# Kernel optimization log

Measured on AMD Instinct MI355X. Metric: run time of the kernel, lower is better.

The kernel has to match this reference:

```python
import jax, jax.numpy as jnp
import numpy as np

N, L, S, E, A, D = 16, 256, 128, 128, 9, 768
ARG_ROLES = 23      # score width = ARG_ROLES + 1
MAX_ARG = 9         # hard-coded max_len_arg in the torch module
N_HID = 768


def setup_inputs() -> dict:
    key = jax.random.key(0)
    ks = jax.random.split(key, 10)
    all_embeddings = jax.random.normal(ks[0], (N, L, D), jnp.float32)
    # last-3-layer BERT attention maps, 12 heads, positive entries
    attn_last3 = jax.random.uniform(ks[1], (3, N, 12, L, L), jnp.float32)
    # per-sample sorted distinct first-subword indices (all positive, full length:
    # the ragged filter idxs>0 then keeps everything -> fixed-shape gather)
    idx_keys = jax.random.split(ks[2], N)
    cand = jnp.arange(1, L - MAX_ARG - 1)
    idxs_to_collect = jax.vmap(
        lambda k: jnp.sort(jax.random.choice(k, cand, (S + 2,), replace=False))
    )(idx_keys).astype(jnp.int32)
    is_triggers = (jax.random.uniform(ks[3], (N, S)) < 0.05).astype(jnp.float32)
    is_triggers = is_triggers.at[:, 0].set(1.0)  # >=1 trigger per sample
    entity_mapping = jax.random.normal(ks[4], (N, S, E), jnp.float32) * 0.05
    arg_weight_matrices = jax.random.normal(ks[5], (N, MAX_ARG, A), jnp.float32) * 0.3
    map_keys = jax.random.split(ks[6], N)
    arg_mapping = jax.vmap(
        lambda k: jax.random.permutation(k, ARG_ROLES + 1)[:A]
    )(map_keys).astype(jnp.int32)
    W1 = jax.random.normal(ks[7], (6 * D, N_HID), jnp.float32) * 0.02
    b1 = jnp.zeros((N_HID,), jnp.float32)
    W2 = jax.random.normal(ks[8], (N_HID, 1), jnp.float32) * 0.02
    b2 = jnp.zeros((1,), jnp.float32)
    return {
        "all_embeddings": all_embeddings,
        "attn_last3": attn_last3,
        "entity_mapping": entity_mapping,
        "arg_weight_matrices": arg_weight_matrices,
        "is_triggers": is_triggers,
        "W1": W1, "b1": b1, "W2": W2, "b2": b2,
        "idxs_to_collect": idxs_to_collect,
        "arg_mapping": arg_mapping,
    }


def reference(all_embeddings, attn_last3, entity_mapping, arg_weight_matrices,
              is_triggers, W1, b1, W2, b2, idxs_to_collect, arg_mapping):
    sqrt_d = jnp.sqrt(jnp.asarray(D, jnp.float32))
    sent_idx = idxs_to_collect[:, :S]                      # [N,S] first-subword ids
    # get_fist_subword_embeddings: ragged gather (full-length here)
    sent_emb = jnp.take_along_axis(all_embeddings, sent_idx[:, :, None], axis=1)  # [N,S,D]
    # arg-type tokens sit right after the second-to-last [SEP]
    arg_pos = idxs_to_collect[:, -2:-1] + 1 + jnp.arange(MAX_ARG)[None, :]        # [N,9]
    arg_raw = jnp.take_along_axis(all_embeddings, arg_pos[:, :, None], axis=1)    # [N,9,D]

    entity_emb = jnp.einsum('nsd,nse->ned', sent_emb, entity_mapping)             # [N,E,D]
    trig = jnp.sum(sent_emb * is_triggers[..., None], axis=1) \
           / jnp.sum(is_triggers, axis=1, keepdims=True)                          # [N,D]
    del trig  # _trigger is computed but unused downstream in the torch forward
    arg_emb = jnp.einsum('nkd,nka->nad', arg_raw, arg_weight_matrices)            # [N,A,D]

    # bi-attention scores (broadcast-mul-sum == contraction over D)
    t2a = jnp.einsum('ned,nad->nea', entity_emb, arg_emb) / sqrt_d
    w = (t2a - 5.0) / 2.0                                                         # [N,E,A]
    token_argAwared = jnp.einsum('nea,nad->ned', w, arg_emb)                      # [N,E,D]
    arg_tokenAwared = jnp.einsum('nea,ned->nad', w, entity_emb)                   # [N,A,D]

    # select_hidden_att for each of the last 3 layers
    att_mean = jnp.mean(attn_last3, axis=2)                                       # [3,N,L,L]
    def sel_layer(a):  # a: [N,L,L] -> row/col gather + row renorm
        s = jax.vmap(lambda m, i: m[i][:, i])(a, sent_idx)                        # [N,S,S]
        return s / (jnp.sum(s, axis=-1, keepdims=True) + 1e-9)
    t2t = (sel_layer(att_mean[0]) + sel_layer(att_mean[1]) + sel_layer(att_mean[2])) / 3.0

    h2h_sent = jnp.einsum('nst,ntd->nsd', t2t, sent_emb)                          # [N,S,D]
    # A_h2h and H_ are projected from sent space (S) to entity space (E)
    A_h2h_e = jnp.einsum('nsd,nse->ned', h2h_sent, entity_mapping)                # [N,E,D]
    H_e = entity_emb                                                              # sent_emb projected == entity_emb

    a2a = jax.nn.softmax(jnp.einsum('nad,nbd->nab', arg_emb, arg_emb), axis=-1)   # [N,A,A]
    u2u = jnp.einsum('nab,nbd->nad', a2a, arg_emb)                                # [N,A,D]

    shp = (N, E, A, D)
    H_    = jnp.broadcast_to(H_e[:, :, None, :], shp)
    U_    = jnp.broadcast_to(arg_emb[:, None, :, :], shp)
    A_h2u = jnp.broadcast_to(token_argAwared[:, :, None, :], shp)
    A_h2h = jnp.broadcast_to(A_h2h_e[:, :, None, :], shp)
    A_u2h = jnp.broadcast_to(arg_tokenAwared[:, None, :, :], shp)
    A_u2u = jnp.broadcast_to(u2u[:, None, :, :], shp)
    latent = jnp.concatenate([H_, U_, A_h2u, A_h2h, A_u2h, A_u2u], axis=-1)       # [N,E,A,6D]

    hid = jax.nn.gelu(latent @ W1 + b1, approximate=False)                        # [N,E,A,768]
    score = (hid @ W2 + b2)[..., 0]                                               # [N,E,A]

    # map_arg_to_ids: scatter each arg slot back to its global role id
    def scatter_one(s, ids):  # s [E,A], ids [A]
        return jnp.full((E, ARG_ROLES + 1), -1e6, jnp.float32).at[:, ids].set(s)
    new_score = jax.vmap(scatter_one)(score, arg_mapping)                         # [N,E,24]
    return new_score
```

## Files before the change

kernel.cpp:

```cpp
#include <hip/hip_runtime.h>
#include <math.h>

namespace {
constexpr int N_ = 16, L_ = 256, S_ = 128, E_ = 128, A_ = 9, D_ = 768, H_ = 768, RO_ = 24;
constexpr int IDXW = 130;
constexpr int W1R = 6 * D_;
constexpr float INV_SQRT_D = 0.03608439182435161f;
constexpr int PESZ = 2048 * 768;
constexpr int PASZ = 144 * 768;
constexpr int GB_T2T    = 0;
constexpr int GB_W1T    = 1024;
constexpr int GB_GATHER = 1888;
constexpr int GB_ENTMAP = 2080;
constexpr int GB_ARGU   = 2112;
constexpr int GB_TOTAL  = 2128;
}

using bshort8 = __attribute__((ext_vector_type(8))) short;
using f32x4v = __attribute__((ext_vector_type(4))) float;

__device__ __forceinline__ unsigned short f2bf(float f) {
    unsigned u = __builtin_bit_cast(unsigned, f);
    return (unsigned short)((u + 0x7fffu + ((u >> 16) & 1u)) >> 16);
}

__device__ __forceinline__ float erf_fast(float x) {
    const float ax = fabsf(x);
    const float t = 1.0f / fmaf(0.3275911f, ax, 1.0f);
    float p = fmaf(1.061405429f, t, -1.453152027f);
    p = fmaf(p, t, 1.421413741f);
    p = fmaf(p, t, -0.284496736f);
    p = fmaf(p, t, 0.254829592f);
    p = p * t;
    const float r = 1.0f - p * __expf(-ax * ax);
    return copysignf(r, x);
}

__device__ __forceinline__ void gemm_body128(const unsigned short* __restrict__ A,
                                             const unsigned short* __restrict__ BT,
                                             int lda, int ldb, int c0, int tid,
                                             short (*As)[40], short (*Bs)[40],
                                             f32x4v acc[2][4]) {
    const int wave = tid >> 6, lane = tid & 63;
    const int row16 = lane & 15, quad = lane >> 4;
    for (int k0 = 0; k0 < S_; k0 += 32) {
#pragma unroll
        for (int i = 0; i < 2; ++i) {
            const int idx = tid + 256 * i;
            const int r = idx >> 2, q = idx & 3;
            *reinterpret_cast<bshort8*>(&As[r][q * 8]) =
                *reinterpret_cast<const bshort8*>(A + (size_t)r * lda + k0 + q * 8);
        }
        {
            const int col = tid >> 2, q = tid & 3;
            *reinterpret_cast<bshort8*>(&Bs[col][q * 8]) =
                *reinterpret_cast<const bshort8*>(BT + (size_t)(c0 + col) * ldb + k0 + q * 8);
        }
        __syncthreads();
        bshort8 a[2], b[4];
#pragma unroll
        for (int mi = 0; mi < 2; ++mi)
            a[mi] = *reinterpret_cast<const bshort8*>(&As[wave * 32 + mi * 16 + row16][quad * 8]);
#pragma unroll
        for (int ni = 0; ni < 4; ++ni)
            b[ni] = *reinterpret_cast<const bshort8*>(&Bs[ni * 16 + row16][quad * 8]);
#pragma unroll
        for (int mi = 0; mi < 2; ++mi)
#pragma unroll
            for (int ni = 0; ni < 4; ++ni)
                acc[mi][ni] = __builtin_amdgcn_mfma_f32_16x16x32_bf16(a[mi], b[ni], acc[mi][ni], 0, 0, 0);
        __syncthreads();
    }
}

__global__ __launch_bounds__(256) void stage1_k(const float* __restrict__ all_emb,
                                                const int* __restrict__ idxs,
                                                const float* __restrict__ ent_map,
                                                const float* __restrict__ W1,
                                                const float* __restrict__ argw,
                                                const float* __restrict__ attn,
                                                unsigned short* __restrict__ sentT,
                                                unsigned short* __restrict__ entmapT,
                                                short* __restrict__ W1t,
                                                unsigned short* __restrict__ t2tT,
                                                float* __restrict__ argE,
                                                unsigned short* __restrict__ argEbf,
                                                unsigned short* __restrict__ u2ubf) {
    __shared__ __align__(16) unsigned char smem[16896];
    const int b = blockIdx.x, tid = threadIdx.x;

    if (b < GB_W1T) {
        const int idx = b - GB_T2T;
        const int n = idx >> 6;
        const int half = tid >> 7, t128 = tid & 127;
        const int s0 = (idx & 63) << 1;
        const int s = s0 | half;
        const int w = t128 >> 6, lane = tid & 63;
        float* sum2 = (float*)smem;
        float* part = (float*)(smem + 12288);
        unsigned short* tileT = (unsigned short*)(smem + 12544);
        const int is = idxs[n * IDXW + s], it = idxs[n * IDXW + t128];
#pragma unroll
        for (int l = 0; l < 3; ++l) {
            const float* base = attn + ((size_t)((l * N_ + n) * 12 + w * 6)) * (L_ * L_)
                              + (size_t)is * L_ + lane * 4;
            float4 acc = {0.f, 0.f, 0.f, 0.f};
#pragma unroll
            for (int h = 0; h < 6; ++h) {
                const float4 v = *reinterpret_cast<const float4*>(base + (size_t)h * (L_ * L_));
                acc.x += v.x; acc.y += v.y; acc.z += v.z; acc.w += v.w;
            }
            *reinterpret_cast<float4*>(&sum2[(((half * 3 + l) * 2 + w) << 8) + lane * 4]) = acc;
        }
        __syncthreads();
        float m[3];
#pragma unroll
        for (int l = 0; l < 3; ++l) {
            m[l] = (sum2[(((half * 3 + l) * 2 + 0) << 8) + it] +
                    sum2[(((half * 3 + l) * 2 + 1) << 8) + it]) * (1.0f / 12.0f);
            float r = m[l];
#pragma unroll
            for (int off = 32; off; off >>= 1) r += __shfl_xor(r, off, 64);
            if (lane == 0) part[(half * 3 + l) * 2 + w] = r;
        }
        __syncthreads();
        float o = 0.f;
#pragma unroll
        for (int l = 0; l < 3; ++l)
            o += m[l] / (part[(half * 3 + l) * 2 + 0] + part[(half * 3 + l) * 2 + 1] + 1e-9f);
        tileT[t128 * 2 + half] = f2bf(o * (1.0f / 3.0f));
        __syncthreads();
        if (tid < 128) {
            const unsigned int v = ((const unsigned int*)tileT)[tid];
            *reinterpret_cast<unsigned int*>(t2tT + ((size_t)(n * S_) + tid) * S_ + s0) = v;
        }
    } else if (b < GB_GATHER) {
        const int b2 = b - GB_W1T;
        const int k0 = (b2 % 72) * 64, h0 = (b2 / 72) * 64;
        auto tile = (float (*)[65])smem;
        const int tx = tid & 63, ty = tid >> 6;
#pragma unroll
        for (int i = 0; i < 16; ++i) {
            const int r = ty + i * 4;
            tile[r][tx] = W1[(size_t)(k0 + r) * H_ + h0 + tx];
        }
        __syncthreads();
#pragma unroll
        for (int i = 0; i < 16; ++i) {
            const int r = ty + i * 4;
            W1t[(size_t)(h0 + r) * W1R + k0 + tx] = (short)f2bf(tile[tx][r]);
        }
    } else if (b < GB_ENTMAP) {
        const int b2 = b - GB_GATHER;
        const int n = b2 / 12, d0 = (b2 % 12) * 64;
        auto tile = (unsigned short (*)[132])smem;
#pragma unroll
        for (int it = 0; it < 8; ++it) {
            const int lin = tid + 256 * it;
            const int s = lin >> 4, dq = (lin & 15) * 4;
            const int row = idxs[n * IDXW + s];
            const float4 v = *reinterpret_cast<const float4*>(all_emb + ((size_t)(n * L_ + row)) * D_ + d0 + dq);
            tile[dq + 0][s] = f2bf(v.x); tile[dq + 1][s] = f2bf(v.y);
            tile[dq + 2][s] = f2bf(v.z); tile[dq + 3][s] = f2bf(v.w);
        }
        __syncthreads();
#pragma unroll
        for (int it = 0; it < 8; ++it) {
            const int lin = tid + 256 * it;
            const int d = lin >> 5, s4 = (lin & 31) * 4;
            ushort4 v = {tile[d][s4], tile[d][s4 + 1], tile[d][s4 + 2], tile[d][s4 + 3]};
            *reinterpret_cast<ushort4*>(sentT + ((size_t)(n * D_) + d0 + d) * S_ + s4) = v;
        }
    } else if (b < GB_ARGU) {
        const int idx = b - GB_ENTMAP;
        const int n = idx >> 1, e0 = (idx & 1) * 64;
        auto tile = (unsigned short (*)[132])smem;
#pragma unroll
        for (int it = 0; it < 8; ++it) {
            const int lin = tid + 256 * it;
            const int s = lin >> 4, eq = (lin & 15) * 4;
            const float4 v = *reinterpret_cast<const float4*>(ent_map + ((size_t)(n * S_ + s)) * E_ + e0 + eq);
            tile[eq + 0][s] = f2bf(v.x); tile[eq + 1][s] = f2bf(v.y);
            tile[eq + 2][s] = f2bf(v.z); tile[eq + 3][s] = f2bf(v.w);
        }
        __syncthreads();
#pragma unroll
        for (int it = 0; it < 8; ++it) {
            const int lin = tid + 256 * it;
            const int e = lin >> 5, s4 = (lin & 31) * 4;
            ushort4 v = {tile[e][s4], tile[e][s4 + 1], tile[e][s4 + 2], tile[e][s4 + 3]};
            *reinterpret_cast<ushort4*>(entmapT + ((size_t)(n * E_) + e0 + e) * S_ + s4) = v;
        }
    } else {
        const int n = b - GB_ARGU;
        auto wsm = (float (*)[A_])smem;
        auto part45 = (float (*)[4])(smem + 512);
        auto Psm = (float (*)[A_])(smem + 1536);
        if (tid < A_ * A_) wsm[tid / A_][tid % A_] = argw[n * A_ * A_ + tid];
        __syncthreads();
        const int p0 = idxs[n * IDXW + S_] + 1;
        float pp[45] = {};
        float vals[3][A_];
#pragma unroll
        for (int c = 0; c < 3; ++c) {
            const int d = tid + 256 * c;
            float raw[A_];
#pragma unroll
            for (int k = 0; k < A_; ++k) raw[k] = all_emb[((size_t)(n * L_ + p0 + k)) * D_ + d];
#pragma unroll
            for (int a = 0; a < A_; ++a) {
                float acc = 0.f;
#pragma unroll
                for (int k = 0; k < A_; ++k) acc = fmaf(raw[k], wsm[k][a], acc);
                vals[c][a] = acc;
                argE[((size_t)(n * A_ + a)) * D_ + d] = acc;
                argEbf[((size_t)(n * A_ + a)) * D_ + d] = f2bf(acc);
            }
            int p = 0;
#pragma unroll
            for (int a = 0; a < A_; ++a)
#pragma unroll
                for (int bb = a; bb < A_; ++bb) pp[p++] += vals[c][a] * vals[c][bb];
        }
        const int lane = tid & 63, wv = tid >> 6;
#pragma unroll
        for (int p = 0; p < 45; ++p) {
            float v = pp[p];
            for (int off = 32; off; off >>= 1) v += __shfl_down(v, off, 64);
            if (lane == 0) part45[p][wv] = v;
        }
        __syncthreads();
        if (tid < 45) part45[tid][0] = part45[tid][0] + part45[tid][1] + part45[tid][2] + part45[tid][3];
        __syncthreads();
        if (tid < A_) {
            const int a = tid;
            float v[A_], mx = -1e30f;
#pragma unroll
            for (int bb = 0; bb < A_; ++bb) {
                const int lo = a < bb ? a : bb, hi = a < bb ? bb : a;
                v[bb] = part45[lo * (19 - lo) / 2 + hi - lo][0];
                mx = fmaxf(mx, v[bb]);
            }
            float sm = 0.f;
#pragma unroll
            for (int bb = 0; bb < A_; ++bb) { v[bb] = expf(v[bb] - mx); sm += v[bb]; }
            const float inv = 1.0f / sm;
#pragma unroll
            for (int bb = 0; bb < A_; ++bb) Psm[a][bb] = v[bb] * inv;
        }
        __syncthreads();
#pragma unroll
        for (int c = 0; c < 3; ++c) {
            const int d = tid + 256 * c;
#pragma unroll
            for (int a = 0; a < A_; ++a) {
                float acc = 0.f;
#pragma unroll
                for (int bb = 0; bb < A_; ++bb) acc = fmaf(Psm[a][bb], vals[c][bb], acc);
                u2ubf[((size_t)(n * A_ + a)) * D_ + d] = f2bf(acc);
            }
        }
    }
}

__global__ __launch_bounds__(256) void gemm_pair_k(const unsigned short* __restrict__ entmapT,
                                                   const unsigned short* __restrict__ sentT,
                                                   const unsigned short* __restrict__ t2tT,
                                                   float* __restrict__ entf,
                                                   unsigned short* __restrict__ entbf,
                                                   unsigned short* __restrict__ M1bf) {
    __shared__ __align__(16) short As[128][40];
    __shared__ __align__(16) short Bs[64][40];
    const int bx = blockIdx.x, tid = threadIdx.x;
    const int wave = tid >> 6, lane = tid & 63;
    const int row16 = lane & 15, quad = lane >> 4;
    f32x4v acc[2][4] = {};
    if (bx < 192) {
        const int n = bx / 12, c0 = (bx % 12) * 64;
        gemm_body128(entmapT + (size_t)n * S_ * S_, sentT + (size_t)n * D_ * S_,
                     S_, S_, c0, tid, As, Bs, acc);
#pragma unroll
        for (int mi = 0; mi < 2; ++mi)
#pragma unroll
            for (int ni = 0; ni < 4; ++ni) {
                const int rbase = wave * 32 + mi * 16 + quad * 4;
                const int col = c0 + ni * 16 + row16;
#pragma unroll
                for (int t = 0; t < 4; ++t) {
                    const size_t o = ((size_t)(n * S_) + rbase + t) * D_ + col;
                    entf[o] = acc[mi][ni][t];
                    entbf[o] = f2bf(acc[mi][ni][t]);
                }
            }
    } else {
        const int idx = bx - 192;
        const int n = idx >> 1, c0 = (idx & 1) * 64;
        gemm_body128(entmapT + (size_t)n * S_ * S_, t2tT + (size_t)n * S_ * S_,
                     S_, S_, c0, tid, As, Bs, acc);
#pragma unroll
        for (int mi = 0; mi < 2; ++mi)
#pragma unroll
            for (int ni = 0; ni < 4; ++ni) {
                const int rbase = wave * 32 + mi * 16 + quad * 4;
                const int col = c0 + ni * 16 + row16;
#pragma unroll
                for (int t = 0; t < 4; ++t)
                    M1bf[((size_t)(n * S_) + rbase + t) * S_ + col] = f2bf(acc[mi][ni][t]);
            }
    }
}

__global__ __launch_bounds__(256) void gemm2_k(const unsigned short* __restrict__ M1bf,
                                               const unsigned short* __restrict__ sentT,
                                               const unsigned short* __restrict__ entbf,
                                               const unsigned short* __restrict__ argEbf,
                                               unsigned short* __restrict__ Ah2hbf,
                                               float* __restrict__ wbuf) {
    const int bx = blockIdx.x, tid = threadIdx.x;
    const int wave = tid >> 6, lane = tid & 63;
    const int row16 = lane & 15, quad = lane >> 4;
    if (bx < 192) {
        __shared__ __align__(16) short As[128][40];
        __shared__ __align__(16) short Bs[64][40];
        const int n = bx / 12, c0 = (bx % 12) * 64;
        f32x4v acc[2][4] = {};
        gemm_body128(M1bf + (size_t)n * S_ * S_, sentT + (size_t)n * D_ * S_,
                     S_, S_, c0, tid, As, Bs, acc);
#pragma unroll
        for (int mi = 0; mi < 2; ++mi)
#pragma unroll
            for (int ni = 0; ni < 4; ++ni) {
                const int rbase = wave * 32 + mi * 16 + quad * 4;
                const int col = c0 + ni * 16 + row16;
#pragma unroll
                for (int t = 0; t < 4; ++t)
                    Ah2hbf[((size_t)(n * S_) + rbase + t) * D_ + col] = f2bf(acc[mi][ni][t]);
            }
    } else {
        const int n = bx - 192;
        const unsigned short* Aent = entbf + (size_t)n * E_ * D_;
        const unsigned short* Barg = argEbf + (size_t)n * A_ * D_;
        f32x4v acc[2] = {};
        for (int k0 = 0; k0 < D_; k0 += 32) {
            bshort8 a[2], bb;
#pragma unroll
            for (int mi = 0; mi < 2; ++mi)
                a[mi] = *reinterpret_cast<const bshort8*>(Aent + (size_t)(wave * 32 + mi * 16 + row16) * D_ + k0 + quad * 8);
            bb = *reinterpret_cast<const bshort8*>(Barg + (size_t)row16 * D_ + k0 + quad * 8);
#pragma unroll
            for (int mi = 0; mi < 2; ++mi)
                acc[mi] = __builtin_amdgcn_mfma_f32_16x16x32_bf16(a[mi], bb, acc[mi], 0, 0, 0);
        }
        if (row16 < A_) {
#pragma unroll
            for (int mi = 0; mi < 2; ++mi)
#pragma unroll
                for (int t = 0; t < 4; ++t) {
                    const int e = wave * 32 + mi * 16 + quad * 4 + t;
                    const float w = (acc[mi][t] * INV_SQRT_D - 5.0f) * 0.5f;
                    wbuf[((size_t)(n * E_ + e)) * A_ + row16] = w;
                }
        }
    }
}

__global__ __launch_bounds__(256) void post_k(const float* __restrict__ wbuf,
                                              const float* __restrict__ argE,
                                              const float* __restrict__ entf,
                                              unsigned short* __restrict__ tokAbf,
                                              unsigned short* __restrict__ argTbf) {
    const int b = blockIdx.x, tid = threadIdx.x;
    if (b < N_ * E_) {
        const int n = b >> 7, e = b & 127;
        __shared__ float wl[A_];
        if (tid < A_) wl[tid] = wbuf[(size_t)(n * E_ + e) * A_ + tid];
        __syncthreads();
        const float* ar = argE + (size_t)n * A_ * D_;
#pragma unroll
        for (int c = 0; c < 3; ++c) {
            const int d = tid + 256 * c;
            float s = 0.f;
#pragma unroll
            for (int a = 0; a < A_; ++a) s = fmaf(wl[a], ar[(size_t)a * D_ + d], s);
            tokAbf[((size_t)(n * E_ + e)) * D_ + d] = f2bf(s);
        }
    } else {
        const int idx = b - N_ * E_;
        const int n = idx / A_, a = idx % A_;
        __shared__ float wl[E_];
        if (tid < E_) wl[tid] = wbuf[(size_t)(n * E_ + tid) * A_ + a];
        __syncthreads();
        const float* eb = entf + (size_t)n * E_ * D_;
#pragma unroll
        for (int c = 0; c < 3; ++c) {
            const int d = tid + 256 * c;
            float acc = 0.f;
            for (int e = 0; e < E_; ++e) acc = fmaf(wl[e], eb[(size_t)e * D_ + d], acc);
            argTbf[((size_t)(n * A_ + a)) * D_ + d] = f2bf(acc);
        }
    }
}

__global__ __launch_bounds__(256) void mfma_mlp_k(const unsigned short* __restrict__ e0,
                                                  const unsigned short* __restrict__ e1,
                                                  const unsigned short* __restrict__ e2,
                                                  const unsigned short* __restrict__ a0,
                                                  const unsigned short* __restrict__ a1,
                                                  const unsigned short* __restrict__ a2,
                                                  const short* __restrict__ W1t,
                                                  float* __restrict__ Pe3, float* __restrict__ Pa3) {
    __shared__ __align__(16) short As[128][40];
    __shared__ __align__(16) short Bs[64][40];
    const int bx = blockIdx.x;
    const int seg = bx % 3;
    const int blk = bx / 3;
    const bool isPa = blk >= 16;
    const unsigned short* Aseg;
    int woff;
    if (isPa) {
        Aseg = seg == 0 ? a0 : (seg == 1 ? a1 : a2);
        woff = seg == 0 ? 1 * D_ : (seg == 1 ? 4 * D_ : 5 * D_);
    } else {
        Aseg = seg == 0 ? e0 : (seg == 1 ? e1 : e2);
        woff = seg == 0 ? 0 : (seg == 1 ? 2 * D_ : 3 * D_);
    }
    const int M = isPa ? N_ * A_ : N_ * E_;
    const int r0 = (isPa ? blk - 16 : blk) * 128;
    float* C = isPa ? (Pa3 + (size_t)seg * PASZ) : (Pe3 + (size_t)seg * PESZ);
    const int c0 = blockIdx.y * 64;
    const int tid = threadIdx.x;
    const int wave = tid >> 6, lane = tid & 63;
    const int row16 = lane & 15, quad = lane >> 4;
    f32x4v acc[2][4] = {};
    for (int kk = 0; kk < D_; kk += 32) {
#pragma unroll
        for (int i = 0; i < 2; ++i) {
            const int idx = tid + 256 * i;
            const int r = idx >> 2, q = idx & 3;
            bshort8 av = {};
            if (r0 + r < M) av = *reinterpret_cast<const bshort8*>(Aseg + (size_t)(r0 + r) * D_ + kk + q * 8);
            *reinterpret_cast<bshort8*>(&As[r][q * 8]) = av;
        }
        {
            const int col = tid >> 2, q = tid & 3;
            *reinterpret_cast<bshort8*>(&Bs[col][q * 8]) =
                *reinterpret_cast<const bshort8*>(W1t + (size_t)(c0 + col) * W1R + woff + kk + q * 8);
        }
        __syncthreads();
        bshort8 a[2], b[4];
#pragma unroll
        for (int mi = 0; mi < 2; ++mi)
            a[mi] = *reinterpret_cast<const bshort8*>(&As[wave * 32 + mi * 16 + row16][quad * 8]);
#pragma unroll
        for (int ni = 0; ni < 4; ++ni)
            b[ni] = *reinterpret_cast<const bshort8*>(&Bs[ni * 16 + row16][quad * 8]);
#pragma unroll
        for (int mi = 0; mi < 2; ++mi)
#pragma unroll
            for (int ni = 0; ni < 4; ++ni)
                acc[mi][ni] = __builtin_amdgcn_mfma_f32_16x16x32_bf16(a[mi], b[ni], acc[mi][ni], 0, 0, 0);
        __syncthreads();
    }
#pragma unroll
    for (int mi = 0; mi < 2; ++mi) {
#pragma unroll
        for (int ni = 0; ni < 4; ++ni) {
            const int rbase = r0 + wave * 32 + mi * 16 + quad * 4;
            const int col = c0 + ni * 16 + row16;
#pragma unroll
            for (int t = 0; t < 4; ++t)
                if (rbase + t < M) C[(size_t)(rbase + t) * H_ + col] = acc[mi][ni][t];
        }
    }
}

__global__ __launch_bounds__(256) void score_k(const float* __restrict__ Pe3, const float* __restrict__ Pa3,
                                               const float* __restrict__ b1, const float* __restrict__ W2,
                                               const float* __restrict__ b2, const int* __restrict__ arg_map,
                                               float* __restrict__ out) {
    const int n = blockIdx.x >> 7, e = blockIdx.x & 127;
    const int tid = threadIdx.x;
    __shared__ float paS[A_ * H_];
    __shared__ float part[A_][4];
    float* orow = out + ((size_t)(n * E_ + e)) * RO_;
    if (tid < RO_) orow[tid] = -1000000.0f;
    for (int i = tid; i < A_ * H_; i += 256) {
        const size_t o = (size_t)n * A_ * H_ + i;
        paS[i] = Pa3[o] + Pa3[PASZ + o] + Pa3[2 * PASZ + o];
    }
    __syncthreads();
    const size_t ro = ((size_t)(n * E_ + e)) * H_;
    float acc[A_] = {};
    for (int h = tid; h < H_; h += 256) {
        const float pe = Pe3[ro + h] + Pe3[PESZ + ro + h] + Pe3[2 * PESZ + ro + h] + b1[h];
        const float w2 = W2[h];
#pragma unroll
        for (int a = 0; a < A_; ++a) {
            const float x = pe + paS[a * H_ + h];
            const float g = x * 0.5f * (1.0f + erf_fast(x * 0.70710678118654752f));
            acc[a] = fmaf(g, w2, acc[a]);
        }
    }
    const int lane = tid & 63, wv = tid >> 6;
#pragma unroll
    for (int a = 0; a < A_; ++a)
        for (int off = 32; off; off >>= 1) acc[a] += __shfl_down(acc[a], off, 64);
    if (lane == 0)
        for (int a = 0; a < A_; ++a) part[a][wv] = acc[a];
    __syncthreads();
    if (tid < A_) {
        const float s = part[tid][0] + part[tid][1] + part[tid][2] + part[tid][3] + b2[0];
        orow[arg_map[n * A_ + tid]] = s;
    }
}

extern "C" void kernel_launch(void* const* d_in, const int* in_sizes, int n_in,
                              void* d_out, int out_size, void* d_ws, size_t ws_size,
                              hipStream_t stream) {
    const float* all_emb = (const float*)d_in[0];
    const float* attn    = (const float*)d_in[1];
    const float* ent_map = (const float*)d_in[2];
    const float* argw    = (const float*)d_in[3];
    const float* W1 = (const float*)d_in[5];
    const float* b1 = (const float*)d_in[6];
    const float* W2 = (const float*)d_in[7];
    const float* b2 = (const float*)d_in[8];
    const int* idxs    = (const int*)d_in[9];
    const int* arg_map = (const int*)d_in[10];
    float* out = (float*)d_out;

    float* ws = (float*)d_ws;
    float* entf = ws + 0;
    float* Pe3  = ws + 1572864;
    float* argE = ws + 6291456;
    float* wbuf = ws + 6402048;
    float* Pa3  = ws + 6420480;
    short*          W1t     = (short*)(ws + 6752256);
    unsigned short* sentT   = (unsigned short*)(ws + 8521728);
    unsigned short* entmapT = (unsigned short*)(ws + 9308160);
    unsigned short* t2tT    = (unsigned short*)(ws + 9439232);
    unsigned short* M1bf    = (unsigned short*)(ws + 9570304);
    unsigned short* argEbf  = (unsigned short*)(ws + 9701376);
    unsigned short* u2ubf   = (unsigned short*)(ws + 9756672);
    unsigned short* entbf   = (unsigned short*)(ws + 9811968);
    unsigned short* Ah2hbf  = (unsigned short*)(ws + 10598400);
    unsigned short* tokAbf  = (unsigned short*)(ws + 11384832);
    unsigned short* argTbf  = (unsigned short*)(ws + 12171264);

    stage1_k<<<GB_TOTAL, 256, 0, stream>>>(all_emb, idxs, ent_map, W1, argw, attn,
                                           sentT, entmapT, W1t, t2tT, argE, argEbf, u2ubf);

    gemm_pair_k<<<224, 256, 0, stream>>>(entmapT, sentT, t2tT, entf, entbf, M1bf);

    gemm2_k<<<208, 256, 0, stream>>>(M1bf, sentT, entbf, argEbf, Ah2hbf, wbuf);

    post_k<<<N_ * E_ + N_ * A_, 256, 0, stream>>>(wbuf, argE, entf, tokAbf, argTbf);

    mfma_mlp_k<<<dim3(54, H_ / 64), 256, 0, stream>>>(entbf, tokAbf, Ah2hbf, argEbf, argTbf, u2ubf, W1t, Pe3, Pa3);

    score_k<<<N_ * E_, 256, 0, stream>>>(Pe3, Pa3, b1, W2, b2, arg_map, out);

    (void)in_sizes; (void)n_in; (void)out_size; (void)ws_size;
}
```

Measured before the change: 319.8 us.

## Reassociate token-arg-aware MLP term to avoid materializing tokA activations

The token_argAwared segment was built as wbuf @ argE per entity and then multiplied by its W1 slice in a large GEMM. It is now reassociated as wbuf @ (argE @ W1_slice). The small argE·W1 product is computed in extra gemm_pair blocks, and the 9-term correction is folded into the epilogue of the entity GEMM. This removes the tokA write and read, one third of the entity-side MLP GEMM work, the fp32 argE buffer, and one Pe partial buffer in score_k. In exchange it adds a naive un-tiled MFMA loop reading global memory directly and changes the bf16 rounding points.

```diff
diff --git a/kernel.cpp b/kernel.cpp
--- a/kernel.cpp
+++ b/kernel.cpp
@@ -83,7 +83,6 @@
                                                 unsigned short* __restrict__ entmapT,
                                                 short* __restrict__ W1t,
                                                 unsigned short* __restrict__ t2tT,
-                                                float* __restrict__ argE,
                                                 unsigned short* __restrict__ argEbf,
                                                 unsigned short* __restrict__ u2ubf) {
     __shared__ __align__(16) unsigned char smem[16896];
@@ -213,7 +212,6 @@
 #pragma unroll
                 for (int k = 0; k < A_; ++k) acc = fmaf(raw[k], wsm[k][a], acc);
                 vals[c][a] = acc;
-                argE[((size_t)(n * A_ + a)) * D_ + d] = acc;
                 argEbf[((size_t)(n * A_ + a)) * D_ + d] = f2bf(acc);
             }
             int p = 0;
@@ -266,17 +264,20 @@
 __global__ __launch_bounds__(256) void gemm_pair_k(const unsigned short* __restrict__ entmapT,
                                                    const unsigned short* __restrict__ sentT,
                                                    const unsigned short* __restrict__ t2tT,
+                                                   const unsigned short* __restrict__ argEbf,
+                                                   const short* __restrict__ W1t,
                                                    float* __restrict__ entf,
                                                    unsigned short* __restrict__ entbf,
-                                                   unsigned short* __restrict__ M1bf) {
+                                                   unsigned short* __restrict__ M1bf,
+                                                   float* __restrict__ argEW2) {
     __shared__ __align__(16) short As[128][40];
     __shared__ __align__(16) short Bs[64][40];
     const int bx = blockIdx.x, tid = threadIdx.x;
     const int wave = tid >> 6, lane = tid & 63;
     const int row16 = lane & 15, quad = lane >> 4;
-    f32x4v acc[2][4] = {};
     if (bx < 192) {
         const int n = bx / 12, c0 = (bx % 12) * 64;
+        f32x4v acc[2][4] = {};
         gemm_body128(entmapT + (size_t)n * S_ * S_, sentT + (size_t)n * D_ * S_,
                      S_, S_, c0, tid, As, Bs, acc);
 #pragma unroll
@@ -292,9 +293,10 @@
                     entbf[o] = f2bf(acc[mi][ni][t]);
                 }
             }
-    } else {
+    } else if (bx < 224) {
         const int idx = bx - 192;
         const int n = idx >> 1, c0 = (idx & 1) * 64;
+        f32x4v acc[2][4] = {};
         gemm_body128(entmapT + (size_t)n * S_ * S_, t2tT + (size_t)n * S_ * S_,
                      S_, S_, c0, tid, As, Bs, acc);
 #pragma unroll
@@ -307,6 +309,26 @@
                 for (int t = 0; t < 4; ++t)
                     M1bf[((size_t)(n * S_) + rbase + t) * S_ + col] = f2bf(acc[mi][ni][t]);
             }
+    } else {
+        const int n = bx - 224;
+        const unsigned short* Ar = argEbf + (size_t)n * A_ * D_;
+        const unsigned short* BT = (const unsigned short*)W1t + (size_t)2 * D_;
+        float* outp = argEW2 + (size_t)n * A_ * H_;
+#pragma unroll
+        for (int i = 0; i < 12; ++i) {
+            const int col0 = (wave * 12 + i) * 16;
+            f32x4v acc = {};
+            for (int k0 = 0; k0 < D_; k0 += 32) {
+                bshort8 a8 = *reinterpret_cast<const bshort8*>(Ar + (size_t)row16 * D_ + k0 + quad * 8);
+                bshort8 b8 = *reinterpret_cast<const bshort8*>(BT + (size_t)(col0 + row16) * W1R + k0 + quad * 8);
+                acc = __builtin_amdgcn_mfma_f32_16x16x32_bf16(a8, b8, acc, 0, 0, 0);
+            }
+#pragma unroll
+            for (int t = 0; t < 4; ++t) {
+                const int a = quad * 4 + t;
+                if (a < A_) outp[(size_t)a * H_ + col0 + row16] = acc[t];
+            }
+        }
     }
 }
 
@@ -364,70 +386,56 @@
     }
 }
 
-__global__ __launch_bounds__(256) void post_k(const float* __restrict__ wbuf,
-                                              const float* __restrict__ argE,
+__global__ __launch_bounds__(256) void argT_k(const float* __restrict__ wbuf,
                                               const float* __restrict__ entf,
-                                              unsigned short* __restrict__ tokAbf,
                                               unsigned short* __restrict__ argTbf) {
-    const int b = blockIdx.x, tid = threadIdx.x;
-    if (b < N_ * E_) {
-        const int n = b >> 7, e = b & 127;
-        __shared__ float wl[A_];
-        if (tid < A_) wl[tid] = wbuf[(size_t)(n * E_ + e) * A_ + tid];
-        __syncthreads();
-        const float* ar = argE + (size_t)n * A_ * D_;
-#pragma unroll
-        for (int c = 0; c < 3; ++c) {
-            const int d = tid + 256 * c;
-            float s = 0.f;
-#pragma unroll
-            for (int a = 0; a < A_; ++a) s = fmaf(wl[a], ar[(size_t)a * D_ + d], s);
-            tokAbf[((size_t)(n * E_ + e)) * D_ + d] = f2bf(s);
-        }
-    } else {
-        const int idx = b - N_ * E_;
-        const int n = idx / A_, a = idx % A_;
-        __shared__ float wl[E_];
-        if (tid < E_) wl[tid] = wbuf[(size_t)(n * E_ + tid) * A_ + a];
-        __syncthreads();
-        const float* eb = entf + (size_t)n * E_ * D_;
-#pragma unroll
-        for (int c = 0; c < 3; ++c) {
-            const int d = tid + 256 * c;
-            float acc = 0.f;
-            for (int e = 0; e < E_; ++e) acc = fmaf(wl[e], eb[(size_t)e * D_ + d], acc);
-            argTbf[((size_t)(n * A_ + a)) * D_ + d] = f2bf(acc);
-        }
-    }
-}
-
-__global__ __launch_bounds__(256) void mfma_mlp_k(const unsigned short* __restrict__ e0,
-                                                  const unsigned short* __restrict__ e1,
-                                                  const unsigned short* __restrict__ e2,
-                                                  const unsigned short* __restrict__ a0,
-                                                  const unsigned short* __restrict__ a1,
-                                                  const unsigned short* __restrict__ a2,
+    const int n = blockIdx.x / A_, a = blockIdx.x % A_;
+    const int tid = threadIdx.x;
+    __shared__ float wl[E_];
+    if (tid < E_) wl[tid] = wbuf[(size_t)(n * E_ + tid) * A_ + a];
+    __syncthreads();
+    const float* eb = entf + (size_t)n * E_ * D_;
+#pragma unroll
+    for (int c = 0; c < 3; ++c) {
+        const int d = tid + 256 * c;
+        float acc = 0.f;
+        for (int e = 0; e < E_; ++e) acc = fmaf(wl[e], eb[(size_t)e * D_ + d], acc);
+        argTbf[((size_t)(n * A_ + a)) * D_ + d] = f2bf(acc);
+    }
+}
+
+__global__ __launch_bounds__(256) void mfma_mlp_k(const unsigned short* __restrict__ entbf,
+                                                  const unsigned short* __restrict__ Ah2hbf,
+                                                  const unsigned short* __restrict__ argEbf,
+                                                  const unsigned short* __restrict__ argTbf,
+                                                  const unsigned short* __restrict__ u2ubf,
                                                   const short* __restrict__ W1t,
-                                                  float* __restrict__ Pe3, float* __restrict__ Pa3) {
+                                                  const float* __restrict__ wbuf,
+                                                  const float* __restrict__ argEW2,
+                                                  float* __restrict__ Pe2, float* __restrict__ Pa3) {
     __shared__ __align__(16) short As[128][40];
     __shared__ __align__(16) short Bs[64][40];
     const int bx = blockIdx.x;
-    const int seg = bx % 3;
-    const int blk = bx / 3;
-    const bool isPa = blk >= 16;
+    const int c0 = blockIdx.y * 64;
+    const bool isPe = bx < 32;
+    int seg, blk, M, woff;
     const unsigned short* Aseg;
-    int woff;
-    if (isPa) {
-        Aseg = seg == 0 ? a0 : (seg == 1 ? a1 : a2);
+    float* C;
+    if (isPe) {
+        seg = bx >> 4; blk = bx & 15;
+        Aseg = seg == 0 ? entbf : Ah2hbf;
+        woff = seg == 0 ? 0 : 3 * D_;
+        M = N_ * E_;
+        C = Pe2 + (size_t)seg * PESZ;
+    } else {
+        const int q = bx - 32;
+        seg = q >> 1; blk = q & 1;
+        Aseg = seg == 0 ? argEbf : (seg == 1 ? argTbf : u2ubf);
         woff = seg == 0 ? 1 * D_ : (seg == 1 ? 4 * D_ : 5 * D_);
-    } else {
-        Aseg = seg == 0 ? e0 : (seg == 1 ? e1 : e2);
-        woff = seg == 0 ? 0 : (seg == 1 ? 2 * D_ : 3 * D_);
-    }
-    const int M = isPa ? N_ * A_ : N_ * E_;
-    const int r0 = (isPa ? blk - 16 : blk) * 128;
-    float* C = isPa ? (Pa3 + (size_t)seg * PASZ) : (Pe3 + (size_t)seg * PESZ);
-    const int c0 = blockIdx.y * 64;
+        M = N_ * A_;
+        C = Pa3 + (size_t)seg * PASZ;
+    }
+    const int r0 = blk * 128;
     const int tid = threadIdx.x;
     const int wave = tid >> 6, lane = tid & 63;
     const int row16 = lane & 15, quad = lane >> 4;
@@ -461,20 +469,40 @@
                 acc[mi][ni] = __builtin_amdgcn_mfma_f32_16x16x32_bf16(a[mi], b[ni], acc[mi][ni], 0, 0, 0);
         __syncthreads();
     }
+    float* wS = (float*)As;
+    float* aW2 = (float*)Bs;
+    if (isPe && seg == 0) {
+        const int n = blk;
+        for (int i = tid; i < E_ * A_; i += 256) wS[i] = wbuf[(size_t)n * E_ * A_ + i];
+        for (int i = tid; i < A_ * 64; i += 256)
+            aW2[i] = argEW2[((size_t)(n * A_) + (i >> 6)) * H_ + c0 + (i & 63)];
+        __syncthreads();
+    }
 #pragma unroll
     for (int mi = 0; mi < 2; ++mi) {
 #pragma unroll
         for (int ni = 0; ni < 4; ++ni) {
-            const int rbase = r0 + wave * 32 + mi * 16 + quad * 4;
+            const int lrow = wave * 32 + mi * 16 + quad * 4;
             const int col = c0 + ni * 16 + row16;
 #pragma unroll
-            for (int t = 0; t < 4; ++t)
-                if (rbase + t < M) C[(size_t)(rbase + t) * H_ + col] = acc[mi][ni][t];
-        }
-    }
-}
-
-__global__ __launch_bounds__(256) void score_k(const float* __restrict__ Pe3, const float* __restrict__ Pa3,
+            for (int t = 0; t < 4; ++t) {
+                const int g = r0 + lrow + t;
+                if (g < M) {
+                    float v = acc[mi][ni][t];
+                    if (isPe && seg == 0) {
+                        const int e = lrow + t;
+#pragma unroll
+                        for (int a = 0; a < A_; ++a)
+                            v = fmaf(wS[e * A_ + a], aW2[a * 64 + ni * 16 + row16], v);
+                    }
+                    C[(size_t)g * H_ + col] = v;
+                }
+            }
+        }
+    }
+}
+
+__global__ __launch_bounds__(256) void score_k(const float* __restrict__ Pe2, const float* __restrict__ Pa3,
                                                const float* __restrict__ b1, const float* __restrict__ W2,
                                                const float* __restrict__ b2, const int* __restrict__ arg_map,
                                                float* __restrict__ out) {
@@ -492,7 +520,7 @@
     const size_t ro = ((size_t)(n * E_ + e)) * H_;
     float acc[A_] = {};
     for (int h = tid; h < H_; h += 256) {
-        const float pe = Pe3[ro + h] + Pe3[PESZ + ro + h] + Pe3[2 * PESZ + ro + h] + b1[h];
+        const float pe = Pe2[ro + h] + Pe2[PESZ + ro + h] + b1[h];
         const float w2 = W2[h];
 #pragma unroll
         for (int a = 0; a < A_; ++a) {
@@ -530,35 +558,36 @@
     float* out = (float*)d_out;
 
     float* ws = (float*)d_ws;
-    float* entf = ws + 0;
-    float* Pe3  = ws + 1572864;
-    float* argE = ws + 6291456;
-    float* wbuf = ws + 6402048;
-    float* Pa3  = ws + 6420480;
-    short*          W1t     = (short*)(ws + 6752256);
-    unsigned short* sentT   = (unsigned short*)(ws + 8521728);
-    unsigned short* entmapT = (unsigned short*)(ws + 9308160);
-    unsigned short* t2tT    = (unsigned short*)(ws + 9439232);
-    unsigned short* M1bf    = (unsigned short*)(ws + 9570304);
-    unsigned short* argEbf  = (unsigned short*)(ws + 9701376);
-    unsigned short* u2ubf   = (unsigned short*)(ws + 9756672);
-    unsigned short* entbf   = (unsigned short*)(ws + 9811968);
-    unsigned short* Ah2hbf  = (unsigned short*)(ws + 10598400);
-    unsigned short* tokAbf  = (unsigned short*)(ws + 11384832);
-    unsigned short* argTbf  = (unsigned short*)(ws + 12171264);
+    float* entf   = ws + 0;
+    float* Pe2    = ws + 1572864;
+    float* wbuf   = ws + 4718592;
+    float* Pa3    = ws + 4737024;
+    float* argEW2 = ws + 5068800;
+    short*          W1t     = (short*)(ws + 5179392);
+    unsigned short* sentT   = (unsigned short*)(ws + 6948864);
+    unsigned short* entmapT = (unsigned short*)(ws + 7735296);
+    unsigned short* t2tT    = (unsigned short*)(ws + 7866368);
+    unsigned short* M1bf    = (unsigned short*)(ws + 7997440);
+    unsigned short* argEbf  = (unsigned short*)(ws + 8128512);
+    unsigned short* u2ubf   = (unsigned short*)(ws + 8183808);
+    unsigned short* entbf   = (unsigned short*)(ws + 8239104);
+    unsigned short* Ah2hbf  = (unsigned short*)(ws + 8632320);
+    unsigned short* argTbf  = (unsigned short*)(ws + 9025536);
 
     stage1_k<<<GB_TOTAL, 256, 0, stream>>>(all_emb, idxs, ent_map, W1, argw, attn,
-                                           sentT, entmapT, W1t, t2tT, argE, argEbf, u2ubf);
-
-    gemm_pair_k<<<224, 256, 0, stream>>>(entmapT, sentT, t2tT, entf, entbf, M1bf);
+                                           sentT, entmapT, W1t, t2tT, argEbf, u2ubf);
+
+    gemm_pair_k<<<240, 256, 0, stream>>>(entmapT, sentT, t2tT, argEbf, W1t,
+                                         entf, entbf, M1bf, argEW2);
 
     gemm2_k<<<208, 256, 0, stream>>>(M1bf, sentT, entbf, argEbf, Ah2hbf, wbuf);
 
-    post_k<<<N_ * E_ + N_ * A_, 256, 0, stream>>>(wbuf, argE, entf, tokAbf, argTbf);
-
-    mfma_mlp_k<<<dim3(54, H_ / 64), 256, 0, stream>>>(entbf, tokAbf, Ah2hbf, argEbf, argTbf, u2ubf, W1t, Pe3, Pa3);
-
-    score_k<<<N_ * E_, 256, 0, stream>>>(Pe3, Pa3, b1, W2, b2, arg_map, out);
+    argT_k<<<N_ * A_, 256, 0, stream>>>(wbuf, entf, argTbf);
+
+    mfma_mlp_k<<<dim3(38, H_ / 64), 256, 0, stream>>>(entbf, Ah2hbf, argEbf, argTbf, u2ubf,
+                                                      W1t, wbuf, argEW2, Pe2, Pa3);
+
+    score_k<<<N_ * E_, 256, 0, stream>>>(Pe2, Pa3, b1, W2, b2, arg_map, out);
 
     (void)in_sizes; (void)n_in; (void)out_size; (void)ws_size;
 }
```

Result: slower. 373.0 us (+16.6%).
